# Optimization experiments

Hardware: AMD Instinct MI355X
Metric: run time of the kernel (lower is better)

The kernel has to match this reference:

```python
import jax, jax.numpy as jnp
import numpy as np

KS = 3; PAD = 1; NK = KS * KS  # 3x3 deform kernel, 9 sampling points

def conv2d(x, w, b=None, pad=1):
    out = jax.lax.conv_general_dilated(x, w, (1, 1), [(pad, pad), (pad, pad)],
                                       dimension_numbers=('NCHW', 'OIHW', 'NCHW'))
    return out if b is None else out + b[None, :, None, None]

def bn(x, g, b, m, v, eps=1e-5):
    s = g * jax.lax.rsqrt(v + eps)
    return x * s[None, :, None, None] + (b - m * s)[None, :, None, None]

def pool2(x, kind):
    if kind == 'max':
        return jax.lax.reduce_window(x, -jnp.inf, jax.lax.max, (1, 1, 2, 2), (1, 1, 2, 2), 'VALID')
    s = jax.lax.reduce_window(x, 0.0, jax.lax.add, (1, 1, 2, 2), (1, 1, 2, 2), 'VALID')
    return s * 0.25

def _gather(xflat, idx):
    # xflat [b,c,Hp*Wp], idx [b,h,w,NK] int32 -> [b,c,h,w,NK]
    b, c, _ = xflat.shape
    out = jax.vmap(lambda xf, ix: xf[:, ix])(xflat, idx.reshape(b, -1))
    return out.reshape(b, c, *idx.shape[1:])

def deform_conv(x, pw, pb, w):
    # DeformConv2D: internal offset conv -> bilinear gather -> 3x3-equivalent conv (einsum)
    b, c, h, wd = x.shape
    off = conv2d(x, pw, pb).transpose(0, 2, 3, 1)  # [b,h,w,2*NK], first NK = x(row), last NK = y(col)
    rng = jnp.arange(KS, dtype=x.dtype) - (KS - 1) // 2
    pn_x = jnp.repeat(rng, KS)  # kernel row offsets, n = 3*i + j ordering
    pn_y = jnp.tile(rng, KS)
    px = jnp.arange(1, h + 1, dtype=x.dtype)[:, None, None] + pn_x + off[..., :NK]  # [b,h,w,NK]
    py = jnp.arange(1, wd + 1, dtype=x.dtype)[None, :, None] + pn_y + off[..., NK:]
    Hp, Wp = h + 2 * PAD, wd + 2 * PAD
    px = jnp.clip(px, 0, Hp - 1); py = jnp.clip(py, 0, Wp - 1)
    x0 = jnp.clip(jnp.floor(px), 0, Hp - 1); y0 = jnp.clip(jnp.floor(py), 0, Wp - 1)
    x1 = jnp.clip(x0 + 1, 0, Hp - 1);        y1 = jnp.clip(y0 + 1, 0, Wp - 1)
    g_lt = (1 + x0 - px) * (1 + y0 - py)
    g_rb = (1 - x1 + px) * (1 - y1 + py)
    g_lb = (1 + x0 - px) * (1 - y1 + py)
    g_rt = (1 - x1 + px) * (1 + y0 - py)
    xp = jnp.pad(x, ((0, 0), (0, 0), (PAD, PAD), (PAD, PAD))).reshape(b, c, Hp * Wp)
    ix0 = x0.astype(jnp.int32); iy0 = y0.astype(jnp.int32)
    ix1 = x1.astype(jnp.int32); iy1 = y1.astype(jnp.int32)
    v = (g_lt[:, None] * _gather(xp, ix0 * Wp + iy0)
       + g_rb[:, None] * _gather(xp, ix1 * Wp + iy1)
       + g_lb[:, None] * _gather(xp, ix0 * Wp + iy1)
       + g_rt[:, None] * _gather(xp, ix1 * Wp + iy0))  # [b,c,h,w,NK]
    oc = w.shape[0]
    return jnp.einsum('bchwn,ocn->bohw', v, w.reshape(oc, c, NK))

def reference(x, d1_pw, d1_pb, d1_w, bn1_g, bn1_b, bn1_m, bn1_v,
              c2_w, c2_b, bn2_g, bn2_b, bn2_m, bn2_v,
              d3_pw, d3_pb, d3_w, bn3_g, bn3_b, bn3_m, bn3_v,
              c4_w, c4_b, bn4_g, bn4_b, bn4_m, bn4_v,
              c5_w, c5_b, bn5_g, bn5_b, bn5_m, bn5_v,
              c6_w, c6_b, bn6_g, bn6_b, bn6_m, bn6_v,
              fc_w, fc_b, fc1_w, fc1_b):
    h = jax.nn.relu(bn(deform_conv(x, d1_pw, d1_pb, d1_w), bn1_g, bn1_b, bn1_m, bn1_v))
    h = pool2(jax.nn.relu(bn(conv2d(h, c2_w, c2_b), bn2_g, bn2_b, bn2_m, bn2_v)), 'max')
    h = jax.nn.relu(bn(deform_conv(h, d3_pw, d3_pb, d3_w), bn3_g, bn3_b, bn3_m, bn3_v))  # Dropout(0.1) eval = id
    h = pool2(jax.nn.relu(bn(conv2d(h, c4_w, c4_b), bn4_g, bn4_b, bn4_m, bn4_v)), 'max')
    h = jax.nn.relu(bn(conv2d(h, c5_w, c5_b), bn5_g, bn5_b, bn5_m, bn5_v))
    h = pool2(jax.nn.relu(bn(conv2d(h, c6_w, c6_b), bn6_g, bn6_b, bn6_m, bn6_v)), 'avg')
    h = h.reshape(h.shape[0], -1)  # [b, 128*2*2]
    h = h @ fc_w.T + fc_b          # Dropout eval = id
    return h @ fc1_w.T + fc1_b

def setup_inputs():
    key = jax.random.key(0)
    keys = iter(jax.random.split(key, 80))
    nk = lambda: next(keys)
    B, C, P, NC = 128, 200, 16, 16
    d = {}
    d['x'] = jax.random.normal(nk(), (B, C, P, P), jnp.float32)
    def conv_w(oc, ic, k=3, scale=None):
        s = scale if scale is not None else 1.0 / np.sqrt(ic * k * k)
        return jax.random.normal(nk(), (oc, ic, k, k), jnp.float32) * s
    def add_bn(name, c):
        d[name + '_g'] = 1.0 + 0.1 * jax.random.normal(nk(), (c,), jnp.float32)
        d[name + '_b'] = 0.1 * jax.random.normal(nk(), (c,), jnp.float32)
        d[name + '_m'] = 0.1 * jax.random.normal(nk(), (c,), jnp.float32)
        d[name + '_v'] = jax.random.uniform(nk(), (c,), jnp.float32) + 0.5
    d['d1_pw'] = conv_w(2 * NK, C, scale=0.01); d['d1_pb'] = jnp.zeros(2 * NK, jnp.float32)
    d['d1_w'] = conv_w(96, C); add_bn('bn1', 96)
    d['c2_w'] = conv_w(96, 96); d['c2_b'] = jnp.zeros(96, jnp.float32); add_bn('bn2', 96)
    d['d3_pw'] = conv_w(2 * NK, 96, scale=0.01); d['d3_pb'] = jnp.zeros(2 * NK, jnp.float32)
    d['d3_w'] = conv_w(108, 96); add_bn('bn3', 108)
    d['c4_w'] = conv_w(108, 108); d['c4_b'] = jnp.zeros(108, jnp.float32); add_bn('bn4', 108)
    d['c5_w'] = conv_w(128, 108); d['c5_b'] = jnp.zeros(128, jnp.float32); add_bn('bn5', 128)
    d['c6_w'] = conv_w(128, 128); d['c6_b'] = jnp.zeros(128, jnp.float32); add_bn('bn6', 128)
    d['fc_w'] = jax.random.normal(nk(), (200, 512), jnp.float32) / np.sqrt(512)
    d['fc_b'] = jnp.zeros(200, jnp.float32)
    d['fc1_w'] = jax.random.normal(nk(), (NC, 200), jnp.float32) / np.sqrt(200)
    d['fc1_b'] = jnp.zeros(NC, jnp.float32)
    return d
```

## Files before the change

### kernel.cpp

```cpp
#include <hip/hip_runtime.h>

typedef __attribute__((ext_vector_type(8))) short short8;
typedef __attribute__((ext_vector_type(4))) float f32x4;

#define MFMA16(a, b, c) __builtin_amdgcn_mfma_f32_16x16x32_bf16(a, b, c, 0, 0, 0)

__device__ __forceinline__ unsigned short f2bf(float x) {
  union { float f; unsigned u; } c; c.f = x;
  unsigned r = c.u + 0x7FFFu + ((c.u >> 16) & 1u);
  return (unsigned short)(r >> 16);
}
__device__ __forceinline__ float bf2f(unsigned short h) {
  union { unsigned u; float f; } c; c.u = ((unsigned)h) << 16; return c.f;
}
__device__ __forceinline__ unsigned cvtpk(float lo, float hi) {
  unsigned r;
  asm("v_cvt_pk_bf16_f32 %0, %1, %2" : "=v"(r) : "v"(lo), "v"(hi));
  return r;
}

static constexpr size_t PK_D1PW = 0;
static constexpr size_t PK_D1W  = 237568;
static constexpr size_t PK_C2W  = 950272;
static constexpr size_t PK_D3PW = 1294336;
static constexpr size_t PK_D3W  = 1409024;
static constexpr size_t PK_C4W  = 1810432;
static constexpr size_t OFF1_B  = 2269184;
static constexpr size_t H2P_B   = 2269184;
static constexpr size_t H1_B    = 5414912;
static constexpr size_t OFF3_B  = 5414912;
static constexpr size_t H3_B    = 5709824;
static constexpr size_t H4P_B   = 9248768;
static constexpr size_t H5_B    = 10133504;
static constexpr size_t H6P_B   = 11182080;
static constexpr size_t FCO_B   = 11444224;
static constexpr size_t PT5_B   = 11546624;
static constexpr size_t PT6_B   = 12044288;

__global__ __launch_bounds__(256) void k_pack6(
    const float* __restrict__ s0, const float* __restrict__ s1,
    const float* __restrict__ s2, const float* __restrict__ s3,
    const float* __restrict__ s4, const float* __restrict__ s5,
    char* __restrict__ ws) {
  int blk = blockIdx.x;
  const float* src; unsigned short* dst; int K, Kp, OC, IC; bool gm;
  if      (blk <  232) { src=s0; dst=(unsigned short*)(ws+PK_D1PW); OC=18;  K=1800; Kp=1856; IC=200; gm=false; }
  else if (blk <  952) { src=s1; dst=(unsigned short*)(ws+PK_D1W);  OC=96;  K=1800; Kp=1920; IC=200; gm=true;  blk -= 232; }
  else if (blk < 1288) { src=s2; dst=(unsigned short*)(ws+PK_C2W);  OC=96;  K=864;  Kp=896;  IC=96;  gm=false; blk -= 952; }
  else if (blk < 1400) { src=s3; dst=(unsigned short*)(ws+PK_D3PW); OC=18;  K=864;  Kp=896;  IC=96;  gm=false; blk -= 1288; }
  else if (blk < 1792) { src=s4; dst=(unsigned short*)(ws+PK_D3W);  OC=108; K=864;  Kp=896;  IC=96;  gm=true;  blk -= 1400; }
  else                 { src=s5; dst=(unsigned short*)(ws+PK_C4W);  OC=108; K=972;  Kp=1024; IC=108; gm=false; blk -= 1792; }
  int e = blk * 256 + threadIdx.x;
  int oc = e / Kp, k = e - oc * Kp;
  float v = 0.f;
  if (oc < OC) {
    if (gm) {
      int NCB = (IC + 15) >> 4;
      if (k < NCB * 144) {
        int cb = k / 144, r = k - cb*144;
        int n = r >> 4, ci = cb*16 + (r & 15);
        if (ci < IC) v = src[(size_t)oc*K + ci*9 + n];
      }
    } else {
      if (k < K) v = src[(size_t)oc*K + k];
    }
  }
  dst[e] = f2bf(v);
}

__global__ __launch_bounds__(256) void k_packT(
    const float* __restrict__ s5, const float* __restrict__ s6,
    char* __restrict__ ws) {
  int e = blockIdx.x * 256 + threadIdx.x;
  if (e < 124416) {
    int k = e >> 7, oc = e & 127;
    ((float*)(ws + PT5_B))[e] = s5[(size_t)oc*972 + k];
  } else if (e < 124416 + 147456) {
    int e2 = e - 124416;
    int k = e2 >> 7, oc = e2 & 127;
    ((float*)(ws + PT6_B))[e2] = s6[(size_t)oc*1152 + k];
  }
}

template<int IC, int OC, int OCPAD, int NT, int H, int W, bool ROLLING>
__global__ __launch_bounds__(256, 2) void k_dgemm(
    const float* __restrict__ in,
    const unsigned short* __restrict__ offb,
    const unsigned short* __restrict__ wpk,
    const float* __restrict__ bng, const float* __restrict__ bnb,
    const float* __restrict__ bnm, const float* __restrict__ bnv,
    float* __restrict__ out) {
  constexpr int HW   = H * W;
  constexpr int NCB  = (IC + 15) >> 4;
  constexpr int KV   = NCB * 144;
  constexpr int NP   = (KV + 63) / 64;
  constexpr int KPAD = NP * 64;
  constexpr int TILES = HW / 64;
  constexpr int HP = H + 2, WPD = W + 2;
  constexpr int BSZ = OCPAD * 64 * 2;
  constexpr int CHUNKF = HW * 16;
  constexpr int SLOTS  = ROLLING ? 2 : NCB;
  constexpr int XSZ    = SLOTS * CHUNKF * 4;
  constexpr int TIDX = 576 * 4, TWT = 576 * 16;
  constexpr int PBYTES = TIDX + TWT + BSZ + XSZ;
  constexpr int NBV = (OCPAD * 8 + 255) / 256;
  __shared__ __align__(16) char pool[PBYTES];
  uchar4* s_idx = (uchar4*)pool;
  float4* s_wt  = (float4*)(pool + TIDX);
  unsigned short* s_bh = (unsigned short*)(pool + TIDX + TWT);
  float* s_xt = (float*)(pool + TIDX + TWT + BSZ);

  const int tid = threadIdx.x;
  const int b   = blockIdx.x / TILES;
  const int hw0 = (blockIdx.x % TILES) * 64;
  const float* __restrict__ inb = in + (size_t)b * IC * HW;

  for (int i = tid; i < 576; i += 256) {
    int px2 = i / 9, n = i % 9;
    int h = (hw0 + px2) / W, w = (hw0 + px2) % W;
    float offx = bf2f(offb[(((size_t)b*18 + n)*HW) + h*W + w]);
    float offy = bf2f(offb[(((size_t)b*18 + 9 + n)*HW) + h*W + w]);
    float pxv = (float)(h + n/3) + offx;
    float pyv = (float)(w + n%3) + offy;
    pxv = fminf(fmaxf(pxv, 0.f), (float)(HP - 1));
    pyv = fminf(fmaxf(pyv, 0.f), (float)(WPD - 1));
    float x0 = floorf(pxv), y0 = floorf(pyv);
    float x1 = fminf(x0 + 1.f, (float)(HP - 1));
    float y1 = fminf(y0 + 1.f, (float)(WPD - 1));
    float glt = (1.f + x0 - pxv) * (1.f + y0 - pyv);
    float grb = (1.f - x1 + pxv) * (1.f - y1 + pyv);
    float glb = (1.f + x0 - pxv) * (1.f - y1 + pyv);
    float grt = (1.f - x1 + pxv) * (1.f + y0 - pyv);
    int   cx[4] = {(int)x0, (int)x1, (int)x0, (int)x1};
    int   cy[4] = {(int)y0, (int)y1, (int)y1, (int)y0};
    float gw[4] = {glt, grb, glb, grt};
    unsigned char id[4]; float gg[4];
#pragma unroll
    for (int q = 0; q < 4; ++q) {
      bool ok = (cx[q] >= 1) && (cx[q] <= H) && (cy[q] >= 1) && (cy[q] <= W);
      id[q] = ok ? (unsigned char)((cx[q]-1)*W + (cy[q]-1)) : (unsigned char)0;
      gg[q] = ok ? gw[q] : 0.f;
    }
    s_idx[i] = make_uchar4(id[0], id[1], id[2], id[3]);
    s_wt[i]  = make_float4(gg[0], gg[1], gg[2], gg[3]);
  }

  auto stageX = [&](int cb) {
    const int slot = ROLLING ? (cb & 1) : cb;
    float* dst = s_xt + (size_t)slot * CHUNKF;
    if constexpr (HW == 256) {
      const int pp = tid;
#pragma unroll
      for (int qj = 0; qj < 4; ++qj) {
        float4 v4;
#pragma unroll
        for (int i2 = 0; i2 < 4; ++i2) {
          int ci = cb*16 + qj*4 + i2;
          ((float*)&v4)[i2] = (ci < IC) ? inb[(size_t)ci*HW + pp] : 0.f;
        }
        *(float4*)(dst + pp*16 + ((((pp >> 1) + qj) & 3) << 2)) = v4;
      }
    } else {
      const int pp = tid & 63;
      const int qj = tid >> 6;
      float4 v4;
#pragma unroll
      for (int i2 = 0; i2 < 4; ++i2) {
        int ci = cb*16 + qj*4 + i2;
        ((float*)&v4)[i2] = (ci < IC) ? inb[(size_t)ci*HW + pp] : 0.f;
      }
      *(float4*)(dst + pp*16 + ((((pp >> 1) + qj) & 3) << 2)) = v4;
    }
  };
  if (ROLLING) stageX(0);
  else { for (int cb = 0; cb < NCB; ++cb) stageX(cb); }
  int staged = 0;

  const int lane = tid & 63;
  const int wv   = tid >> 6;
  const int m16  = lane & 15;
  const int quad = lane >> 4;
  const int pv   = wv*16 + m16;
  const int tbase = pv * 9;
  f32x4 acc[NT];
#pragma unroll
  for (int nt = 0; nt < NT; ++nt) acc[nt] = (f32x4){0.f, 0.f, 0.f, 0.f};
  short8 rb[NBV];

  auto prefB = [&](int p) {
    if (p >= NP) return;
    const int k0 = p * 64;
#pragma unroll
    for (int j = 0; j < NBV; ++j) {
      int e = tid + 256*j;
      if (e < OCPAD*8) {
        int oc = e >> 3, kq = e & 7;
        rb[j] = *(const short8*)(wpk + (size_t)oc*KPAD + k0 + kq*8);
      }
    }
  };
  auto commitB = [&]() {
#pragma unroll
    for (int j = 0; j < NBV; ++j) {
      int e = tid + 256*j;
      if (e < OCPAD*8) {
        int oc = e >> 3, kq = e & 7;
        *(short8*)&s_bh[(kq*OCPAD + (oc ^ ((kq*2)&7)))*8] = rb[j];
      }
    }
  };

  auto buildA = [&](int kk, short8& ahv, short8& alv) {
    float v[8];
    if (kk < KV) {
      const int cb2 = kk / 144;
      const int rem = kk - cb2*144;
      const int n   = rem >> 4;
      const int g0  = (rem >> 2) & 2;
      const int slot = ROLLING ? (cb2 & 1) : cb2;
      const float* xb = s_xt + (size_t)slot * CHUNKF;
      uchar4 t4 = s_idx[tbase + n];
      float4 w4 = s_wt[tbase + n];
      const int r0i = (int)t4.x, r1i = (int)t4.y;
      const int r2i = (int)t4.z, r3i = (int)t4.w;
      const float* r0 = xb + r0i * 16;
      const float* r1 = xb + r1i * 16;
      const float* r2 = xb + r2i * 16;
      const float* r3 = xb + r3i * 16;
      float4 A0[2], A1[2], A2[2], A3[2];
#pragma unroll
      for (int j = 0; j < 2; ++j) {
        A0[j] = *(const float4*)(r0 + ((((r0i >> 1) + g0 + j) & 3) << 2));
        A1[j] = *(const float4*)(r1 + ((((r1i >> 1) + g0 + j) & 3) << 2));
        A2[j] = *(const float4*)(r2 + ((((r2i >> 1) + g0 + j) & 3) << 2));
        A3[j] = *(const float4*)(r3 + ((((r3i >> 1) + g0 + j) & 3) << 2));
      }
#pragma unroll
      for (int j = 0; j < 2; ++j) {
        v[4*j+0] = w4.x*A0[j].x + w4.y*A1[j].x + w4.z*A2[j].x + w4.w*A3[j].x;
        v[4*j+1] = w4.x*A0[j].y + w4.y*A1[j].y + w4.z*A2[j].y + w4.w*A3[j].y;
        v[4*j+2] = w4.x*A0[j].z + w4.y*A1[j].z + w4.z*A2[j].z + w4.w*A3[j].z;
        v[4*j+3] = w4.x*A0[j].w + w4.y*A1[j].w + w4.z*A2[j].w + w4.w*A3[j].w;
      }
    } else {
#pragma unroll
      for (int i = 0; i < 8; ++i) v[i] = 0.f;
    }
    unsigned hp[4], lp[4];
#pragma unroll
    for (int i = 0; i < 4; ++i) {
      unsigned h = cvtpk(v[2*i], v[2*i+1]);
      float h0 = __uint_as_float(h << 16);
      float h1 = __uint_as_float(h & 0xFFFF0000u);
      hp[i] = h;
      lp[i] = cvtpk(v[2*i] - h0, v[2*i+1] - h1);
    }
    uint4 uh = make_uint4(hp[0], hp[1], hp[2], hp[3]);
    uint4 ul = make_uint4(lp[0], lp[1], lp[2], lp[3]);
    ahv = *(short8*)&uh;
    alv = *(short8*)&ul;
  };

  prefB(0);
  __syncthreads();

  for (int p = 0; p < NP; ++p) {
    short8 ah[2], al[2];
    buildA(p*64 +      quad*8, ah[0], al[0]);
    buildA(p*64 + 32 + quad*8, ah[1], al[1]);
    commitB();
    if (ROLLING) {
      int want = ((p + 1) * 64 + 63) / 144;
      if (want >= NCB) want = NCB - 1;
      if (want > staged) { stageX(want); staged = want; }
    }
    prefB(p + 1);
    __syncthreads();
#pragma unroll
    for (int ks = 0; ks < 2; ++ks) {
      const int kg = ks*4 + quad;
      const int xm = (kg*2) & 7;
#pragma unroll
      for (int nt = 0; nt < NT; ++nt) {
        short8 bh = *(const short8*)&s_bh[(kg*OCPAD + ((nt*16 + m16) ^ xm))*8];
        acc[nt] = MFMA16(ah[ks], bh, acc[nt]);
        acc[nt] = MFMA16(al[ks], bh, acc[nt]);
      }
    }
    __syncthreads();
  }

#pragma unroll
  for (int nt = 0; nt < NT; ++nt) {
    int oc = nt*16 + m16;
    if (oc < OC) {
      float sc = bng[oc] * rsqrtf(bnv[oc] + 1e-5f);
      float sh = bnb[oc] - bnm[oc] * sc;
#pragma unroll
      for (int reg = 0; reg < 4; ++reg) {
        int rowl = wv*16 + quad*4 + reg;
        float e = fmaxf(acc[nt][reg] * sc + sh, 0.f);
        out[((size_t)b*OC + oc)*HW + hw0 + rowl] = e;
      }
    }
  }
}

template<int IC, int OC, int OCPAD, int NT, int H, int W,
         bool HASBIAS, bool HASBN, bool RELU, int OUTMODE, int MINW, bool ALO>
__global__ __launch_bounds__(256, MINW) void k_gemm(
    const float* __restrict__ in,
    const unsigned short* __restrict__ wpk,
    const float* __restrict__ bias,
    const float* __restrict__ bng, const float* __restrict__ bnb,
    const float* __restrict__ bnm, const float* __restrict__ bnv,
    void* __restrict__ outv) {
  constexpr int HW   = H * W;
  constexpr int K    = IC * 9;
  constexpr int NP   = (K + 63) / 64;
  constexpr int KPAD = NP * 64;
  constexpr int TILES = HW / 64;
  constexpr int BSZ = OCPAD * 64 * 2;
  constexpr int SXS = HW + 8;
  constexpr int SXSZ = 8 * SXS * 4;
  constexpr int CPT = HW / 32;
  constexpr int PBST = BSZ + 2*SXSZ;
  constexpr int SOUTB = (OUTMODE == 2) ? 64 * (OC + 1) * 4 : 0;
  constexpr int PBYTES = (PBST > SOUTB) ? PBST : SOUTB;
  constexpr int NBV = (OCPAD * 8 + 255) / 256;
  __shared__ __align__(16) char pool[PBYTES];
  unsigned short* s_bh = (unsigned short*)pool;
  float* s_x  = (float*)(pool + BSZ);
  float* s_out = (float*)pool;

  const int tid = threadIdx.x;
  const int b   = blockIdx.x / TILES;
  const int hw0 = (blockIdx.x % TILES) * 64;
  const float* __restrict__ inb = in + (size_t)b * IC * HW;

  const int lane = tid & 63;
  const int wv   = tid >> 6;
  const int m16  = lane & 15;
  const int quad = lane >> 4;
  const int pv   = wv*16 + m16;
  const int hwp  = hw0 + pv;
  const int pr   = hwp / W, pc = hwp % W;
  const int xpl  = tid >> 5;
  const int xo   = (tid & 31) * CPT;
  f32x4 acc[NT];
#pragma unroll
  for (int nt = 0; nt < NT; ++nt) acc[nt] = (f32x4){0.f, 0.f, 0.f, 0.f};

  float  rx[2][CPT];
  short8 rb[NBV];

  auto ci0_of = [&](int p) { int c = (p*64)/9; return (c > IC-8) ? IC-8 : c; };
  auto prefX = [&](int p) {
    if (p >= NP) return;
    const float* s = inb + (size_t)(ci0_of(p) + xpl)*HW + xo;
    if constexpr (CPT == 8) {
      float4 a = ((const float4*)s)[0], c = ((const float4*)s)[1];
      rx[p&1][0]=a.x; rx[p&1][1]=a.y; rx[p&1][2]=a.z; rx[p&1][3]=a.w;
      rx[p&1][4]=c.x; rx[p&1][5]=c.y; rx[p&1][6]=c.z; rx[p&1][7]=c.w;
    } else {
      float2 a = ((const float2*)s)[0];
      rx[p&1][0]=a.x; rx[p&1][1]=a.y;
    }
  };
  auto commitX = [&](int p) {
    if (p >= NP) return;
    float* d = s_x + (size_t)(p&1)*8*SXS + xpl*SXS + xo;
    if constexpr (CPT == 8) {
      ((float4*)d)[0] = make_float4(rx[p&1][0],rx[p&1][1],rx[p&1][2],rx[p&1][3]);
      ((float4*)d)[1] = make_float4(rx[p&1][4],rx[p&1][5],rx[p&1][6],rx[p&1][7]);
    } else {
      ((float2*)d)[0] = make_float2(rx[p&1][0],rx[p&1][1]);
    }
  };
  auto prefB = [&](int p) {
    if (p >= NP) return;
    const int k0 = p * 64;
#pragma unroll
    for (int j = 0; j < NBV; ++j) {
      int e = tid + 256*j;
      if (e < OCPAD*8) {
        int oc = e >> 3, kq = e & 7;
        rb[j] = *(const short8*)(wpk + (size_t)oc*KPAD + k0 + kq*8);
      }
    }
  };
  auto commitB = [&]() {
#pragma unroll
    for (int j = 0; j < NBV; ++j) {
      int e = tid + 256*j;
      if (e < OCPAD*8) {
        int oc = e >> 3, kq = e & 7;
        *(short8*)&s_bh[(kq*OCPAD + (oc ^ ((kq*2)&7)))*8] = rb[j];
      }
    }
  };

  auto buildV = [&](int kk, const float* xb, int ci0c, float* v) {
    int ci = kk / 9, n = kk - ci*9;
#pragma unroll
    for (int i = 0; i < 8; ++i) {
      float val = 0.f;
      if (kk + i < K) {
        int rr = pr + n/3 - 1, cc = pc + n%3 - 1;
        if (rr >= 0 && rr < H && cc >= 0 && cc < W)
          val = xb[(ci - ci0c)*SXS + rr*W + cc];
      }
      v[i] = val;
      if (++n == 9) { n = 0; ++ci; }
    }
  };

  prefX(0); prefB(0); commitX(0); prefX(1);
  __syncthreads();

  for (int p = 0; p < NP; ++p) {
    const int ci0c = ci0_of(p);
    const float* xb = s_x + (size_t)(p&1)*8*SXS;
    short8 ah[2], al[2];
#pragma unroll
    for (int ks = 0; ks < 2; ++ks) {
      float v[8];
      buildV(p*64 + ks*32 + quad*8, xb, ci0c, v);
      unsigned hp[4], lp[4];
#pragma unroll
      for (int i = 0; i < 4; ++i) {
        unsigned h = cvtpk(v[2*i], v[2*i+1]);
        hp[i] = h;
        if constexpr (ALO) {
          float h0 = __uint_as_float(h << 16);
          float h1 = __uint_as_float(h & 0xFFFF0000u);
          lp[i] = cvtpk(v[2*i] - h0, v[2*i+1] - h1);
        }
      }
      uint4 uh = make_uint4(hp[0], hp[1], hp[2], hp[3]);
      ah[ks] = *(short8*)&uh;
      if constexpr (ALO) {
        uint4 ul = make_uint4(lp[0], lp[1], lp[2], lp[3]);
        al[ks] = *(short8*)&ul;
      }
    }
    commitB();
    commitX(p + 1);
    prefB(p + 1);
    prefX(p + 2);
    __syncthreads();
#pragma unroll
    for (int ks = 0; ks < 2; ++ks) {
      const int kg = ks*4 + quad;
      const int xm = (kg*2) & 7;
#pragma unroll
      for (int nt = 0; nt < NT; ++nt) {
        short8 bh = *(const short8*)&s_bh[(kg*OCPAD + ((nt*16 + m16) ^ xm))*8];
        acc[nt] = MFMA16(ah[ks], bh, acc[nt]);
        if constexpr (ALO) acc[nt] = MFMA16(al[ks], bh, acc[nt]);
      }
    }
    __syncthreads();
  }

  constexpr int OCS = OC + 1;
#pragma unroll
  for (int nt = 0; nt < NT; ++nt) {
    int oc = nt*16 + m16;
    float bi = 0.f, sc = 1.f, sh = 0.f;
    if (oc < OC) {
      if constexpr (HASBIAS) bi = bias[oc];
      if constexpr (HASBN) {
        sc = bng[oc] * rsqrtf(bnv[oc] + 1e-5f);
        sh = bnb[oc] - bnm[oc] * sc;
      }
    }
#pragma unroll
    for (int reg = 0; reg < 4; ++reg) {
      int rowl = wv*16 + quad*4 + reg;
      float e = (acc[nt][reg] + bi) * sc + sh;
      if constexpr (RELU) e = fmaxf(e, 0.f);
      if (oc < OC) {
        if constexpr (OUTMODE == 1) {
          ((unsigned short*)outv)[((size_t)b*OC + oc)*HW + hw0 + rowl] = f2bf(e);
        } else {
          s_out[rowl*OCS + oc] = e;
        }
      }
    }
  }
  if constexpr (OUTMODE == 2) {
    __syncthreads();
    constexpr int PR = (64 / W) / 2, PC = W / 2, CNT = PR * PC * OC;
    const int r0 = hw0 / W;
    float* out = (float*)outv;
    for (int e2 = tid; e2 < CNT; e2 += 256) {
      int oc = e2 % OC, q = e2 / OC, pc2 = q % PC, pr2 = q / PC;
      int base = ((2*pr2)*W + 2*pc2)*OCS + oc;
      float a0 = s_out[base],         a1 = s_out[base + OCS];
      float a2 = s_out[base + W*OCS], a3 = s_out[base + W*OCS + OCS];
      float m = fmaxf(fmaxf(a0, a1), fmaxf(a2, a3));
      out[(((size_t)b*OC + oc)*(H/2) + (r0 >> 1) + pr2)*(W/2) + pc2] = m;
    }
  }
}

template<int IC, int OC, bool POOLAVG>
__global__ __launch_bounds__(256, 4) void k_tail(
    const float* __restrict__ in,
    const float* __restrict__ wt,
    const float* __restrict__ bias,
    const float* __restrict__ bng, const float* __restrict__ bnb,
    const float* __restrict__ bnm, const float* __restrict__ bnv,
    float* __restrict__ out) {
  constexpr int NB = OC / 32;
  __shared__ float s_pad[IC * 36];
  const int tid = threadIdx.x;
  const int b = blockIdx.x / NB;
  const int g = blockIdx.x % NB;
  for (int i = tid; i < IC*36; i += 256) {
    int ci = i / 36, pos = i % 36;
    int rr = pos / 6 - 1, cc = pos % 6 - 1;
    bool ok = (rr >= 0) && (rr < 4) && (cc >= 0) && (cc < 4);
    s_pad[i] = ok ? in[((size_t)b*IC + ci)*16 + rr*4 + cc] : 0.f;
  }
  __syncthreads();
  const int oc = g*32 + (tid >> 3);
  const int p  = tid & 7;
  const int r0 = p >> 1, c0 = (p & 1) * 2;
  float a0 = 0.f, a1 = 0.f;
  const float* wp = wt + oc;
#pragma unroll 2
  for (int ci = 0; ci < IC; ++ci) {
    const float* sp = s_pad + ci*36 + r0*6 + c0;
#pragma unroll
    for (int n = 0; n < 9; ++n) {
      float wv = wp[(size_t)(ci*9 + n)*OC];
      float v0 = sp[(n/3)*6 + (n%3)];
      float v1 = sp[(n/3)*6 + (n%3) + 1];
      a0 = fmaf(wv, v0, a0);
      a1 = fmaf(wv, v1, a1);
    }
  }
  float sc = bng[oc] * rsqrtf(bnv[oc] + 1e-5f);
  float sh = bnb[oc] - bnm[oc]*sc;
  float bi = bias[oc];
  float e0 = fmaxf((a0 + bi)*sc + sh, 0.f);
  float e1 = fmaxf((a1 + bi)*sc + sh, 0.f);
  if constexpr (!POOLAVG) {
    size_t ob = ((size_t)b*OC + oc)*16 + r0*4 + c0;
    out[ob]     = e0;
    out[ob + 1] = e1;
  } else {
    float s = e0 + e1;
    float tot = s + __shfl_xor(s, 2);
    if ((p & 2) == 0) {
      int pr = p >> 2, pc = p & 1;
      out[(size_t)b*512 + oc*4 + pr*2 + pc] = tot * 0.25f;
    }
  }
}

__global__ __launch_bounds__(128) void k_fc(const float* __restrict__ in,
                                            const float* __restrict__ w,
                                            const float* __restrict__ bias,
                                            float* __restrict__ out) {
  int j = blockIdx.x, b = threadIdx.x;
  const float4* ib = (const float4*)(in + (size_t)b*512);
  const float4* wb = (const float4*)(w + (size_t)j*512);
  float acc = bias[j];
  for (int k = 0; k < 128; ++k) {
    float4 a = ib[k], q = wb[k];
    acc = fmaf(a.x, q.x, fmaf(a.y, q.y, fmaf(a.z, q.z, fmaf(a.w, q.w, acc))));
  }
  out[(size_t)b*200 + j] = acc;
}

__global__ __launch_bounds__(128) void k_fc1(const float* __restrict__ in,
                                             const float* __restrict__ w,
                                             const float* __restrict__ bias,
                                             float* __restrict__ out) {
  int j = blockIdx.x, b = threadIdx.x;
  const float4* ib = (const float4*)(in + (size_t)b*200);
  const float4* wb = (const float4*)(w + (size_t)j*200);
  float acc = bias[j];
  for (int k = 0; k < 50; ++k) {
    float4 a = ib[k], q = wb[k];
    acc = fmaf(a.x, q.x, fmaf(a.y, q.y, fmaf(a.z, q.z, fmaf(a.w, q.w, acc))));
  }
  out[(size_t)b*16 + j] = acc;
}

extern "C" void kernel_launch(void* const* d_in, const int* in_sizes, int n_in,
                              void* d_out, int out_size, void* d_ws, size_t ws_size,
                              hipStream_t stream) {
  const float* X    = (const float*)d_in[0];
  const float* D1PW = (const float*)d_in[1];
  const float* D1PB = (const float*)d_in[2];
  const float* D1W  = (const float*)d_in[3];
  const float* BN1G = (const float*)d_in[4];
  const float* BN1B = (const float*)d_in[5];
  const float* BN1M = (const float*)d_in[6];
  const float* BN1V = (const float*)d_in[7];
  const float* C2W  = (const float*)d_in[8];
  const float* C2B  = (const float*)d_in[9];
  const float* BN2G = (const float*)d_in[10];
  const float* BN2B = (const float*)d_in[11];
  const float* BN2M = (const float*)d_in[12];
  const float* BN2V = (const float*)d_in[13];
  const float* D3PW = (const float*)d_in[14];
  const float* D3PB = (const float*)d_in[15];
  const float* D3W  = (const float*)d_in[16];
  const float* BN3G = (const float*)d_in[17];
  const float* BN3B = (const float*)d_in[18];
  const float* BN3M = (const float*)d_in[19];
  const float* BN3V = (const float*)d_in[20];
  const float* C4W  = (const float*)d_in[21];
  const float* C4B  = (const float*)d_in[22];
  const float* BN4G = (const float*)d_in[23];
  const float* BN4B = (const float*)d_in[24];
  const float* BN4M = (const float*)d_in[25];
  const float* BN4V = (const float*)d_in[26];
  const float* C5W  = (const float*)d_in[27];
  const float* C5B  = (const float*)d_in[28];
  const float* BN5G = (const float*)d_in[29];
  const float* BN5B = (const float*)d_in[30];
  const float* BN5M = (const float*)d_in[31];
  const float* BN5V = (const float*)d_in[32];
  const float* C6W  = (const float*)d_in[33];
  const float* C6B  = (const float*)d_in[34];
  const float* BN6G = (const float*)d_in[35];
  const float* BN6B = (const float*)d_in[36];
  const float* BN6M = (const float*)d_in[37];
  const float* BN6V = (const float*)d_in[38];
  const float* FCW  = (const float*)d_in[39];
  const float* FCB  = (const float*)d_in[40];
  const float* FC1W = (const float*)d_in[41];
  const float* FC1B = (const float*)d_in[42];

  char* ws = (char*)d_ws;
  unsigned short* pk_d1pw = (unsigned short*)(ws + PK_D1PW);
  unsigned short* pk_d1w  = (unsigned short*)(ws + PK_D1W);
  unsigned short* pk_c2w  = (unsigned short*)(ws + PK_C2W);
  unsigned short* pk_d3pw = (unsigned short*)(ws + PK_D3PW);
  unsigned short* pk_d3w  = (unsigned short*)(ws + PK_D3W);
  unsigned short* pk_c4w  = (unsigned short*)(ws + PK_C4W);
  unsigned short* off1 = (unsigned short*)(ws + OFF1_B);
  unsigned short* off3 = (unsigned short*)(ws + OFF3_B);
  float* h1   = (float*)(ws + H1_B);
  float* h2p  = (float*)(ws + H2P_B);
  float* h3   = (float*)(ws + H3_B);
  float* h4p  = (float*)(ws + H4P_B);
  float* h5   = (float*)(ws + H5_B);
  float* h6p  = (float*)(ws + H6P_B);
  float* fco  = (float*)(ws + FCO_B);
  float* pt5  = (float*)(ws + PT5_B);
  float* pt6  = (float*)(ws + PT6_B);
  float* outp = (float*)d_out;

  k_pack6<<<2240, 256, 0, stream>>>(D1PW, D1W, C2W, D3PW, D3W, C4W, ws);

  k_gemm<200,18,32,2,16,16,true,false,false,1,3,false><<<512, 256, 0, stream>>>(
      X, pk_d1pw, D1PB, nullptr, nullptr, nullptr, nullptr, off1);
  k_dgemm<200,96,96,6,16,16,true><<<512, 256, 0, stream>>>(
      X, off1, pk_d1w, BN1G, BN1B, BN1M, BN1V, h1);
  k_gemm<96,96,96,6,16,16,true,true,true,2,3,true><<<512, 256, 0, stream>>>(
      h1, pk_c2w, C2B, BN2G, BN2B, BN2M, BN2V, h2p);
  k_packT<<<1062, 256, 0, stream>>>(C5W, C6W, ws);
  k_gemm<96,18,32,2,8,8,true,false,false,1,3,false><<<128, 256, 0, stream>>>(
      h2p, pk_d3pw, D3PB, nullptr, nullptr, nullptr, nullptr, off3);
  k_dgemm<96,108,112,7,8,8,false><<<128, 256, 0, stream>>>(
      h2p, off3, pk_d3w, BN3G, BN3B, BN3M, BN3V, h3);
  k_gemm<108,108,112,7,8,8,true,true,true,2,3,true><<<128, 256, 0, stream>>>(
      h3, pk_c4w, C4B, BN4G, BN4B, BN4M, BN4V, h4p);
  k_tail<108,128,false><<<512, 256, 0, stream>>>(
      h4p, pt5, C5B, BN5G, BN5B, BN5M, BN5V, h5);
  k_tail<128,128,true><<<512, 256, 0, stream>>>(
      h5, pt6, C6B, BN6G, BN6B, BN6M, BN6V, h6p);
  k_fc<<<200, 128, 0, stream>>>(h6p, FCW, FCB, fco);
  k_fc1<<<16, 128, 0, stream>>>(fco, FC1W, FC1B, outp);
}
```

Measured before the change: 485.8 us.

## Load weight fragments straight from global into registers, dropping LDS staging

Both GEMM kernels stop staging the packed bf16 weight tile in shared memory. Each lane now reads its MFMA B fragments directly from global memory into registers at the top of every K step. This removes the LDS store and read traffic, shrinks shared memory use, and drops one barrier per iteration. The cost is that all four waves fetch the same weights from global and cache memory, and the loads are issued only one step ahead of use rather than prefetched a full iteration earlier. In the rolling deform kernel, explicit barriers now guard the X staging, since the per-iteration barriers that used to cover it are gone.

Result: slower. 513.1 us (+5.6%).

```diff
diff --git a/kernel.cpp b/kernel.cpp
--- a/kernel.cpp
+++ b/kernel.cpp
@@ -97,18 +97,15 @@
   constexpr int KPAD = NP * 64;
   constexpr int TILES = HW / 64;
   constexpr int HP = H + 2, WPD = W + 2;
-  constexpr int BSZ = OCPAD * 64 * 2;
   constexpr int CHUNKF = HW * 16;
   constexpr int SLOTS  = ROLLING ? 2 : NCB;
   constexpr int XSZ    = SLOTS * CHUNKF * 4;
   constexpr int TIDX = 576 * 4, TWT = 576 * 16;
-  constexpr int PBYTES = TIDX + TWT + BSZ + XSZ;
-  constexpr int NBV = (OCPAD * 8 + 255) / 256;
+  constexpr int PBYTES = TIDX + TWT + XSZ;
   __shared__ __align__(16) char pool[PBYTES];
   uchar4* s_idx = (uchar4*)pool;
   float4* s_wt  = (float4*)(pool + TIDX);
-  unsigned short* s_bh = (unsigned short*)(pool + TIDX + TWT);
-  float* s_xt = (float*)(pool + TIDX + TWT + BSZ);
+  float* s_xt = (float*)(pool + TIDX + TWT);
 
   const int tid = threadIdx.x;
   const int b   = blockIdx.x / TILES;
@@ -185,29 +182,16 @@
   f32x4 acc[NT];
 #pragma unroll
   for (int nt = 0; nt < NT; ++nt) acc[nt] = (f32x4){0.f, 0.f, 0.f, 0.f};
-  short8 rb[NBV];
-
-  auto prefB = [&](int p) {
-    if (p >= NP) return;
-    const int k0 = p * 64;
-#pragma unroll
-    for (int j = 0; j < NBV; ++j) {
-      int e = tid + 256*j;
-      if (e < OCPAD*8) {
-        int oc = e >> 3, kq = e & 7;
-        rb[j] = *(const short8*)(wpk + (size_t)oc*KPAD + k0 + kq*8);
-      }
-    }
-  };
-  auto commitB = [&]() {
-#pragma unroll
-    for (int j = 0; j < NBV; ++j) {
-      int e = tid + 256*j;
-      if (e < OCPAD*8) {
-        int oc = e >> 3, kq = e & 7;
-        *(short8*)&s_bh[(kq*OCPAD + (oc ^ ((kq*2)&7)))*8] = rb[j];
-      }
-    }
+
+  short8 breg[2][NT];
+  const unsigned short* __restrict__ wbase = wpk + (size_t)m16*KPAD + quad*8;
+  auto loadB = [&](int p) {
+    const unsigned short* wp_ = wbase + p*64;
+#pragma unroll
+    for (int ks = 0; ks < 2; ++ks)
+#pragma unroll
+      for (int nt = 0; nt < NT; ++nt)
+        breg[ks][nt] = *(const short8*)(wp_ + (size_t)(nt*16)*KPAD + ks*32);
   };
 
   auto buildA = [&](int kk, short8& ahv, short8& alv) {
@@ -261,33 +245,30 @@
     alv = *(short8*)&ul;
   };
 
-  prefB(0);
   __syncthreads();
 
   for (int p = 0; p < NP; ++p) {
+    loadB(p);
     short8 ah[2], al[2];
     buildA(p*64 +      quad*8, ah[0], al[0]);
     buildA(p*64 + 32 + quad*8, ah[1], al[1]);
-    commitB();
     if (ROLLING) {
       int want = ((p + 1) * 64 + 63) / 144;
       if (want >= NCB) want = NCB - 1;
-      if (want > staged) { stageX(want); staged = want; }
-    }
-    prefB(p + 1);
-    __syncthreads();
-#pragma unroll
-    for (int ks = 0; ks < 2; ++ks) {
-      const int kg = ks*4 + quad;
-      const int xm = (kg*2) & 7;
+      if (want > staged) {
+        __syncthreads();
+        stageX(want);
+        staged = want;
+        __syncthreads();
+      }
+    }
+#pragma unroll
+    for (int ks = 0; ks < 2; ++ks)
 #pragma unroll
       for (int nt = 0; nt < NT; ++nt) {
-        short8 bh = *(const short8*)&s_bh[(kg*OCPAD + ((nt*16 + m16) ^ xm))*8];
-        acc[nt] = MFMA16(ah[ks], bh, acc[nt]);
-        acc[nt] = MFMA16(al[ks], bh, acc[nt]);
-      }
-    }
-    __syncthreads();
+        acc[nt] = MFMA16(ah[ks], breg[ks][nt], acc[nt]);
+        acc[nt] = MFMA16(al[ks], breg[ks][nt], acc[nt]);
+      }
   }
 
 #pragma unroll
@@ -320,17 +301,14 @@
   constexpr int NP   = (K + 63) / 64;
   constexpr int KPAD = NP * 64;
   constexpr int TILES = HW / 64;
-  constexpr int BSZ = OCPAD * 64 * 2;
   constexpr int SXS = HW + 8;
   constexpr int SXSZ = 8 * SXS * 4;
   constexpr int CPT = HW / 32;
-  constexpr int PBST = BSZ + 2*SXSZ;
+  constexpr int PBST = 2*SXSZ;
   constexpr int SOUTB = (OUTMODE == 2) ? 64 * (OC + 1) * 4 : 0;
   constexpr int PBYTES = (PBST > SOUTB) ? PBST : SOUTB;
-  constexpr int NBV = (OCPAD * 8 + 255) / 256;
   __shared__ __align__(16) char pool[PBYTES];
-  unsigned short* s_bh = (unsigned short*)pool;
-  float* s_x  = (float*)(pool + BSZ);
+  float* s_x  = (float*)pool;
   float* s_out = (float*)pool;
 
   const int tid = threadIdx.x;
@@ -352,7 +330,16 @@
   for (int nt = 0; nt < NT; ++nt) acc[nt] = (f32x4){0.f, 0.f, 0.f, 0.f};
 
   float  rx[2][CPT];
-  short8 rb[NBV];
+  short8 breg[2][NT];
+  const unsigned short* __restrict__ wbase = wpk + (size_t)m16*KPAD + quad*8;
+  auto loadB = [&](int p) {
+    const unsigned short* wp_ = wbase + p*64;
+#pragma unroll
+    for (int ks = 0; ks < 2; ++ks)
+#pragma unroll
+      for (int nt = 0; nt < NT; ++nt)
+        breg[ks][nt] = *(const short8*)(wp_ + (size_t)(nt*16)*KPAD + ks*32);
+  };
 
   auto ci0_of = [&](int p) { int c = (p*64)/9; return (c > IC-8) ? IC-8 : c; };
   auto prefX = [&](int p) {
@@ -377,28 +364,6 @@
       ((float2*)d)[0] = make_float2(rx[p&1][0],rx[p&1][1]);
     }
   };
-  auto prefB = [&](int p) {
-    if (p >= NP) return;
-    const int k0 = p * 64;
-#pragma unroll
-    for (int j = 0; j < NBV; ++j) {
-      int e = tid + 256*j;
-      if (e < OCPAD*8) {
-        int oc = e >> 3, kq = e & 7;
-        rb[j] = *(const short8*)(wpk + (size_t)oc*KPAD + k0 + kq*8);
-      }
-    }
-  };
-  auto commitB = [&]() {
-#pragma unroll
-    for (int j = 0; j < NBV; ++j) {
-      int e = tid + 256*j;
-      if (e < OCPAD*8) {
-        int oc = e >> 3, kq = e & 7;
-        *(short8*)&s_bh[(kq*OCPAD + (oc ^ ((kq*2)&7)))*8] = rb[j];
-      }
-    }
-  };
 
   auto buildV = [&](int kk, const float* xb, int ci0c, float* v) {
     int ci = kk / 9, n = kk - ci*9;
@@ -415,10 +380,11 @@
     }
   };
 
-  prefX(0); prefB(0); commitX(0); prefX(1);
+  prefX(0); commitX(0); prefX(1);
   __syncthreads();
 
   for (int p = 0; p < NP; ++p) {
+    loadB(p);
     const int ci0c = ci0_of(p);
     const float* xb = s_x + (size_t)(p&1)*8*SXS;
     short8 ah[2], al[2];
@@ -444,23 +410,16 @@
         al[ks] = *(short8*)&ul;
       }
     }
-    commitB();
     commitX(p + 1);
-    prefB(p + 1);
     prefX(p + 2);
     __syncthreads();
 #pragma unroll
-    for (int ks = 0; ks < 2; ++ks) {
-      const int kg = ks*4 + quad;
-      const int xm = (kg*2) & 7;
+    for (int ks = 0; ks < 2; ++ks)
 #pragma unroll
       for (int nt = 0; nt < NT; ++nt) {
-        short8 bh = *(const short8*)&s_bh[(kg*OCPAD + ((nt*16 + m16) ^ xm))*8];
-        acc[nt] = MFMA16(ah[ks], bh, acc[nt]);
-        if constexpr (ALO) acc[nt] = MFMA16(al[ks], bh, acc[nt]);
-      }
-    }
-    __syncthreads();
+        acc[nt] = MFMA16(ah[ks], breg[ks][nt], acc[nt]);
+        if constexpr (ALO) acc[nt] = MFMA16(al[ks], breg[ks][nt], acc[nt]);
+      }
   }
 
   constexpr int OCS = OC + 1;
```

## Stage halo-padded channel-blocked input tiles in k_gemm and reorder K dimension

Applied to the files above, without the earlier changes.

Changes the regular conv GEMM kernel so the K dimension is ordered by 16-channel blocks times 9 taps, matching the deformable kernel's packing, and all weight packs use that order. Input is staged per channel block as a halo-padded spatial tile with channels contiguous, so each lane builds its A fragment with two float4 LDS reads instead of eight scalar lookups with bounds checks. Staging now happens only when a new channel block is needed, with extra barriers around it (also added to the rolling deformable path), and the register-prefetched double buffering of input is removed. This can expose global load latency at block boundaries, and padding IC to multiples of 16 adds some wasted MFMA work for IC=200 and 108.

Result: faster. 434.3 us (-10.6%).

```diff
diff --git a/kernel.cpp b/kernel.cpp
--- a/kernel.cpp
+++ b/kernel.cpp
@@ -20,11 +20,11 @@
 }
 
 static constexpr size_t PK_D1PW = 0;
-static constexpr size_t PK_D1W  = 237568;
-static constexpr size_t PK_C2W  = 950272;
-static constexpr size_t PK_D3PW = 1294336;
-static constexpr size_t PK_D3W  = 1409024;
-static constexpr size_t PK_C4W  = 1810432;
+static constexpr size_t PK_D1W  = 122880;
+static constexpr size_t PK_C2W  = 491520;
+static constexpr size_t PK_D3PW = 663552;
+static constexpr size_t PK_D3W  = 720896;
+static constexpr size_t PK_C4W  = 921600;
 static constexpr size_t OFF1_B  = 2269184;
 static constexpr size_t H2P_B   = 2269184;
 static constexpr size_t H1_B    = 5414912;
@@ -43,26 +43,22 @@
     const float* __restrict__ s4, const float* __restrict__ s5,
     char* __restrict__ ws) {
   int blk = blockIdx.x;
-  const float* src; unsigned short* dst; int K, Kp, OC, IC; bool gm;
-  if      (blk <  232) { src=s0; dst=(unsigned short*)(ws+PK_D1PW); OC=18;  K=1800; Kp=1856; IC=200; gm=false; }
-  else if (blk <  952) { src=s1; dst=(unsigned short*)(ws+PK_D1W);  OC=96;  K=1800; Kp=1920; IC=200; gm=true;  blk -= 232; }
-  else if (blk < 1288) { src=s2; dst=(unsigned short*)(ws+PK_C2W);  OC=96;  K=864;  Kp=896;  IC=96;  gm=false; blk -= 952; }
-  else if (blk < 1400) { src=s3; dst=(unsigned short*)(ws+PK_D3PW); OC=18;  K=864;  Kp=896;  IC=96;  gm=false; blk -= 1288; }
-  else if (blk < 1792) { src=s4; dst=(unsigned short*)(ws+PK_D3W);  OC=108; K=864;  Kp=896;  IC=96;  gm=true;  blk -= 1400; }
-  else                 { src=s5; dst=(unsigned short*)(ws+PK_C4W);  OC=108; K=972;  Kp=1024; IC=108; gm=false; blk -= 1792; }
+  const float* src; unsigned short* dst; int K, Kp, OC, IC;
+  if      (blk <  240) { src=s0; dst=(unsigned short*)(ws+PK_D1PW); OC=18;  K=1800; Kp=1920; IC=200; }
+  else if (blk <  960) { src=s1; dst=(unsigned short*)(ws+PK_D1W);  OC=96;  K=1800; Kp=1920; IC=200; blk -= 240; }
+  else if (blk < 1296) { src=s2; dst=(unsigned short*)(ws+PK_C2W);  OC=96;  K=864;  Kp=896;  IC=96;  blk -= 960; }
+  else if (blk < 1408) { src=s3; dst=(unsigned short*)(ws+PK_D3PW); OC=18;  K=864;  Kp=896;  IC=96;  blk -= 1296; }
+  else if (blk < 1800) { src=s4; dst=(unsigned short*)(ws+PK_D3W);  OC=108; K=864;  Kp=896;  IC=96;  blk -= 1408; }
+  else                 { src=s5; dst=(unsigned short*)(ws+PK_C4W);  OC=108; K=972;  Kp=1024; IC=108; blk -= 1800; }
   int e = blk * 256 + threadIdx.x;
   int oc = e / Kp, k = e - oc * Kp;
   float v = 0.f;
   if (oc < OC) {
-    if (gm) {
-      int NCB = (IC + 15) >> 4;
-      if (k < NCB * 144) {
-        int cb = k / 144, r = k - cb*144;
-        int n = r >> 4, ci = cb*16 + (r & 15);
-        if (ci < IC) v = src[(size_t)oc*K + ci*9 + n];
-      }
-    } else {
-      if (k < K) v = src[(size_t)oc*K + k];
+    int NCB = (IC + 15) >> 4;
+    if (k < NCB * 144) {
+      int cb = k / 144, r = k - cb*144;
+      int n = r >> 4, ci = cb*16 + (r & 15);
+      if (ci < IC) v = src[(size_t)oc*K + ci*9 + n];
     }
   }
   dst[e] = f2bf(v);
@@ -272,7 +268,12 @@
     if (ROLLING) {
       int want = ((p + 1) * 64 + 63) / 144;
       if (want >= NCB) want = NCB - 1;
-      if (want > staged) { stageX(want); staged = want; }
+      if (want > staged) {
+        __syncthreads();
+        stageX(want);
+        staged = want;
+        __syncthreads();
+      }
     }
     prefB(p + 1);
     __syncthreads();
@@ -316,26 +317,31 @@
     const float* __restrict__ bnm, const float* __restrict__ bnv,
     void* __restrict__ outv) {
   constexpr int HW   = H * W;
-  constexpr int K    = IC * 9;
-  constexpr int NP   = (K + 63) / 64;
+  constexpr int NCB  = (IC + 15) >> 4;
+  constexpr int KV   = NCB * 144;
+  constexpr int NP   = (KV + 63) / 64;
   constexpr int KPAD = NP * 64;
   constexpr int TILES = HW / 64;
-  constexpr int BSZ = OCPAD * 64 * 2;
-  constexpr int SXS = HW + 8;
-  constexpr int SXSZ = 8 * SXS * 4;
-  constexpr int CPT = HW / 32;
-  constexpr int PBST = BSZ + 2*SXSZ;
+  constexpr int RT   = 64 / W;
+  constexpr int HR   = RT + 2, WPD = W + 2;
+  constexpr int HPOS = HR * WPD;
+  constexpr int SROW = 20;
+  constexpr int CHUNKF = HPOS * SROW;
+  constexpr int XSZ  = 2 * CHUNKF * 4;
+  constexpr int BSZ  = OCPAD * 64 * 2;
+  constexpr int PBST = BSZ + XSZ;
   constexpr int SOUTB = (OUTMODE == 2) ? 64 * (OC + 1) * 4 : 0;
   constexpr int PBYTES = (PBST > SOUTB) ? PBST : SOUTB;
   constexpr int NBV = (OCPAD * 8 + 255) / 256;
   __shared__ __align__(16) char pool[PBYTES];
   unsigned short* s_bh = (unsigned short*)pool;
-  float* s_x  = (float*)(pool + BSZ);
+  float* s_xt  = (float*)(pool + BSZ);
   float* s_out = (float*)pool;
 
   const int tid = threadIdx.x;
   const int b   = blockIdx.x / TILES;
   const int hw0 = (blockIdx.x % TILES) * 64;
+  const int r0  = hw0 / W;
   const float* __restrict__ inb = in + (size_t)b * IC * HW;
 
   const int lane = tid & 63;
@@ -343,40 +349,29 @@
   const int m16  = lane & 15;
   const int quad = lane >> 4;
   const int pv   = wv*16 + m16;
-  const int hwp  = hw0 + pv;
-  const int pr   = hwp / W, pc = hwp % W;
-  const int xpl  = tid >> 5;
-  const int xo   = (tid & 31) * CPT;
+  const int lr   = pv / W, lc = pv % W;
   f32x4 acc[NT];
 #pragma unroll
   for (int nt = 0; nt < NT; ++nt) acc[nt] = (f32x4){0.f, 0.f, 0.f, 0.f};
-
-  float  rx[2][CPT];
   short8 rb[NBV];
 
-  auto ci0_of = [&](int p) { int c = (p*64)/9; return (c > IC-8) ? IC-8 : c; };
-  auto prefX = [&](int p) {
-    if (p >= NP) return;
-    const float* s = inb + (size_t)(ci0_of(p) + xpl)*HW + xo;
-    if constexpr (CPT == 8) {
-      float4 a = ((const float4*)s)[0], c = ((const float4*)s)[1];
-      rx[p&1][0]=a.x; rx[p&1][1]=a.y; rx[p&1][2]=a.z; rx[p&1][3]=a.w;
-      rx[p&1][4]=c.x; rx[p&1][5]=c.y; rx[p&1][6]=c.z; rx[p&1][7]=c.w;
-    } else {
-      float2 a = ((const float2*)s)[0];
-      rx[p&1][0]=a.x; rx[p&1][1]=a.y;
-    }
-  };
-  auto commitX = [&](int p) {
-    if (p >= NP) return;
-    float* d = s_x + (size_t)(p&1)*8*SXS + xpl*SXS + xo;
-    if constexpr (CPT == 8) {
-      ((float4*)d)[0] = make_float4(rx[p&1][0],rx[p&1][1],rx[p&1][2],rx[p&1][3]);
-      ((float4*)d)[1] = make_float4(rx[p&1][4],rx[p&1][5],rx[p&1][6],rx[p&1][7]);
-    } else {
-      ((float2*)d)[0] = make_float2(rx[p&1][0],rx[p&1][1]);
-    }
-  };
+  auto stageX = [&](int cb) {
+    float* dst = s_xt + (size_t)(cb & 1) * CHUNKF;
+    for (int e = tid; e < HPOS * 4; e += 256) {
+      int pos = e >> 2, g = e & 3;
+      int hr = pos / WPD, hc = pos % WPD;
+      int ir = r0 + hr - 1, ic = hc - 1;
+      bool okp = (ir >= 0) && (ir < H) && (ic >= 0) && (ic < W);
+      float4 v4;
+#pragma unroll
+      for (int i2 = 0; i2 < 4; ++i2) {
+        int ci = cb*16 + g*4 + i2;
+        ((float*)&v4)[i2] = (okp && ci < IC) ? inb[(size_t)ci*HW + ir*W + ic] : 0.f;
+      }
+      *(float4*)(dst + (size_t)pos*SROW + g*4) = v4;
+    }
+  };
+
   auto prefB = [&](int p) {
     if (p >= NP) return;
     const int k0 = p * 64;
@@ -400,54 +395,64 @@
     }
   };
 
-  auto buildV = [&](int kk, const float* xb, int ci0c, float* v) {
-    int ci = kk / 9, n = kk - ci*9;
-#pragma unroll
-    for (int i = 0; i < 8; ++i) {
-      float val = 0.f;
-      if (kk + i < K) {
-        int rr = pr + n/3 - 1, cc = pc + n%3 - 1;
-        if (rr >= 0 && rr < H && cc >= 0 && cc < W)
-          val = xb[(ci - ci0c)*SXS + rr*W + cc];
-      }
-      v[i] = val;
-      if (++n == 9) { n = 0; ++ci; }
-    }
-  };
-
-  prefX(0); prefB(0); commitX(0); prefX(1);
+  auto buildV = [&](int kk, short8& ahv, short8& alv) {
+    float v[8];
+    if (kk < KV) {
+      const int cb2 = kk / 144;
+      const int rem = kk - cb2*144;
+      const int n   = rem >> 4;
+      const int g0  = (rem >> 2) & 2;
+      const float* xb = s_xt + (size_t)(cb2 & 1) * CHUNKF;
+      const int hpos = (lr + n/3) * WPD + (lc + n%3);
+      const float* rowp = xb + (size_t)hpos * SROW;
+      float4 a0 = *(const float4*)(rowp + g0*4);
+      float4 a1 = *(const float4*)(rowp + (g0+1)*4);
+      v[0]=a0.x; v[1]=a0.y; v[2]=a0.z; v[3]=a0.w;
+      v[4]=a1.x; v[5]=a1.y; v[6]=a1.z; v[7]=a1.w;
+    } else {
+#pragma unroll
+      for (int i = 0; i < 8; ++i) v[i] = 0.f;
+    }
+    unsigned hp[4], lp[4];
+#pragma unroll
+    for (int i = 0; i < 4; ++i) {
+      unsigned h = cvtpk(v[2*i], v[2*i+1]);
+      hp[i] = h;
+      if constexpr (ALO) {
+        float h0 = __uint_as_float(h << 16);
+        float h1 = __uint_as_float(h & 0xFFFF0000u);
+        lp[i] = cvtpk(v[2*i] - h0, v[2*i+1] - h1);
+      }
+    }
+    uint4 uh = make_uint4(hp[0], hp[1], hp[2], hp[3]);
+    ahv = *(short8*)&uh;
+    if constexpr (ALO) {
+      uint4 ul = make_uint4(lp[0], lp[1], lp[2], lp[3]);
+      alv = *(short8*)&ul;
+    }
+  };
+
+  stageX(0);
+  prefB(0);
+  int staged = 0;
   __syncthreads();
 
   for (int p = 0; p < NP; ++p) {
-    const int ci0c = ci0_of(p);
-    const float* xb = s_x + (size_t)(p&1)*8*SXS;
     short8 ah[2], al[2];
-#pragma unroll
-    for (int ks = 0; ks < 2; ++ks) {
-      float v[8];
-      buildV(p*64 + ks*32 + quad*8, xb, ci0c, v);
-      unsigned hp[4], lp[4];
-#pragma unroll
-      for (int i = 0; i < 4; ++i) {
-        unsigned h = cvtpk(v[2*i], v[2*i+1]);
-        hp[i] = h;
-        if constexpr (ALO) {
-          float h0 = __uint_as_float(h << 16);
-          float h1 = __uint_as_float(h & 0xFFFF0000u);
-          lp[i] = cvtpk(v[2*i] - h0, v[2*i+1] - h1);
-        }
-      }
-      uint4 uh = make_uint4(hp[0], hp[1], hp[2], hp[3]);
-      ah[ks] = *(short8*)&uh;
-      if constexpr (ALO) {
-        uint4 ul = make_uint4(lp[0], lp[1], lp[2], lp[3]);
-        al[ks] = *(short8*)&ul;
-      }
-    }
+    buildV(p*64 +      quad*8, ah[0], al[0]);
+    buildV(p*64 + 32 + quad*8, ah[1], al[1]);
     commitB();
-    commitX(p + 1);
+    {
+      int want = ((p + 1) * 64 + 63) / 144;
+      if (want >= NCB) want = NCB - 1;
+      if (want > staged) {
+        __syncthreads();
+        stageX(want);
+        staged = want;
+        __syncthreads();
+      }
+    }
     prefB(p + 1);
-    prefX(p + 2);
     __syncthreads();
 #pragma unroll
     for (int ks = 0; ks < 2; ++ks) {
@@ -492,7 +497,6 @@
   if constexpr (OUTMODE == 2) {
     __syncthreads();
     constexpr int PR = (64 / W) / 2, PC = W / 2, CNT = PR * PC * OC;
-    const int r0 = hw0 / W;
     float* out = (float*)outv;
     for (int e2 = tid; e2 < CNT; e2 += 256) {
       int oc = e2 % OC, q = e2 / OC, pc2 = q % PC, pr2 = q / PC;
@@ -658,7 +662,7 @@
   float* pt6  = (float*)(ws + PT6_B);
   float* outp = (float*)d_out;
 
-  k_pack6<<<2240, 256, 0, stream>>>(D1PW, D1W, C2W, D3PW, D3W, C4W, ws);
+  k_pack6<<<2248, 256, 0, stream>>>(D1PW, D1W, C2W, D3PW, D3W, C4W, ws);
 
   k_gemm<200,18,32,2,16,16,true,false,false,1,3,false><<<512, 256, 0, stream>>>(
       X, pk_d1pw, D1PB, nullptr, nullptr, nullptr, nullptr, off1);
```
